# Kernel tuning notes

Measured on AMD Instinct MI355X. Metric: run time of the kernel, lower is better.

Reference implementation:

```python
import jax, jax.numpy as jnp
import numpy as np


def _edt2(mask):
    """Exact squared Euclidean distance transform of a bool [H,W] mask.

    Returns, per pixel, the squared distance to the nearest False pixel
    (0 where mask is False) -- same semantics as scipy distance_transform_edt^2.
    Pass 1: 1D nearest-zero distance along axis 0 (two scans).
    Pass 2: exact lower envelope along axis 1 via a vectorized min over columns.
    """
    H, W = mask.shape
    BIG = jnp.float32(H + W)  # 1D distance can never exceed H, acts as +inf

    def step(carry, m_row):  # carry: [W] running distance to last zero
        d = jnp.where(m_row, carry + 1.0, 0.0)
        return d, d

    init = jnp.full((W,), BIG, jnp.float32)
    _, fwd = jax.lax.scan(step, init, mask)
    _, bwd = jax.lax.scan(step, init, mask[::-1])
    g2 = jnp.minimum(fwd, bwd[::-1]) ** 2  # [H,W] squared 1D distances

    k = jnp.arange(W, dtype=jnp.float32)
    sq = (k[:, None] - k[None, :]) ** 2  # [Wj, Wk]
    # dt2[i,j] = min_k (j-k)^2 + g2[i,k]
    return jnp.min(g2[:, None, :] + sq[None, :, :], axis=-1)


def _dist_map(mask):
    # edt(pos) + edt(neg), then squared: cross term is 0 (supports disjoint),
    # so (edt_pos + edt_neg)^2 == edt_pos^2 + edt_neg^2 == edt2(pos) + edt2(neg).
    return _edt2(mask) + _edt2(~mask)


_dist_map_bc = jax.vmap(jax.vmap(_dist_map))  # over [B, C]


def setup_inputs() -> dict:
    key = jax.random.key(0)
    k1, k2 = jax.random.split(key)
    B, C, H, W = 8, 1, 256, 256
    inp = jax.random.normal(k1, (B, C, H, W), dtype=jnp.float32)
    target = jax.random.randint(k2, (B, C, H, W), 0, 2, dtype=jnp.int32)
    return {"inp": inp, "target": target}


def reference(inp, target):
    p = jax.nn.sigmoid(inp.astype(jnp.float32))      # [B,C,H,W]
    t = target.astype(jnp.float32)
    # distance maps computed on thresholded masks (no_grad in original)
    dist = _dist_map_bc(p > 0.5) + _dist_map_bc(t > 0.5)
    pred_error = (t - p) ** 2
    per_sample = jnp.mean(pred_error * dist, axis=(1, 2, 3))  # mean over c,x,y
    return jnp.mean(per_sample)[None]  # shape [1], matching FloatTensor(1)
```

## Files before the change

### kernel.cpp

```cpp
#include <hip/hip_runtime.h>


#define IMG 65536

__device__ __forceinline__ float g2_from_words(unsigned long long z0,
                                               unsigned long long z1,
                                               unsigned long long z2,
                                               unsigned long long z3,
                                               int i) {
    int wi = i >> 6, bi = i & 63;
    unsigned long long lowm  = (~0ULL) >> (63 - bi);
    unsigned long long highm = (~0ULL) << bi;
    unsigned long long z[4] = {z0, z1, z2, z3};

    int lz = -513;
    #pragma unroll
    for (int w = 0; w < 4; ++w) {
        unsigned long long m = z[w];
        if (w == wi) m &= lowm;
        if (w >  wi) m = 0;
        if (m) lz = (w << 6) + 63 - __clzll(m);
    }
    int fz = 768;
    #pragma unroll
    for (int w = 3; w >= 0; --w) {
        unsigned long long m = z[w];
        if (w == wi) m &= highm;
        if (w <  wi) m = 0;
        if (m) fz = (w << 6) + (__ffsll(m) - 1);
    }
    int u = i - lz, d = fz - i;
    float g = (float)(u < d ? u : d);
    return g * g;
}

__global__ __launch_bounds__(256) void build_masks(const float* __restrict__ inp,
                                                   const int* __restrict__ tgt,
                                                   unsigned short* __restrict__ PM,
                                                   float* __restrict__ out) {
    int bid = blockIdx.x;
    int w   = threadIdx.x;
    if (bid == 0 && w == 0) out[0] = 0.0f;

    int src = bid >> 7;
    int b   = (bid >> 4) & 7;
    int wd  = (bid >> 2) & 3;
    int q   = bid & 3;
    int h0  = (wd << 6) + (q << 4);
    int base = b * IMG + (h0 << 8) + w;

    unsigned int word = 0;
    if (src == 0) {
        #pragma unroll
        for (int hh = 0; hh < 16; ++hh)
            word |= ((unsigned int)(inp[base + (hh << 8)] > 0.0f)) << hh;
    } else {
        #pragma unroll
        for (int hh = 0; hh < 16; ++hh)
            word |= ((unsigned int)(tgt[base + (hh << 8)] > 0)) << hh;
    }
    PM[((((size_t)src * 8 + b) * 4 + wd) * 256 + w) * 4 + q] = (unsigned short)word;
}

__global__ __launch_bounds__(256) void envelope(const float* __restrict__ inp,
                                                const int* __restrict__ tgt,
                                                const unsigned long long* __restrict__ BM,
                                                float* __restrict__ out) {
    __shared__ float4 sg2[4][256];
    __shared__ float wsum[4];

    int b  = blockIdx.x >> 6;
    int r0 = (blockIdx.x & 63) << 2;
    int t  = threadIdx.x;

    {
        unsigned long long bp[4], bt[4];
        #pragma unroll
        for (int wd = 0; wd < 4; ++wd) {
            bp[wd] = BM[(((size_t)0 * 8 + b) * 4 + wd) * 256 + t];
            bt[wd] = BM[(((size_t)1 * 8 + b) * 4 + wd) * 256 + t];
        }
        #pragma unroll
        for (int rr = 0; rr < 4; ++rr) {
            int i = r0 + rr;
            float g0 = g2_from_words(~bp[0], ~bp[1], ~bp[2], ~bp[3], i);
            float g1 = g2_from_words( bp[0],  bp[1],  bp[2],  bp[3], i);
            float g2 = g2_from_words(~bt[0], ~bt[1], ~bt[2], ~bt[3], i);
            float g3 = g2_from_words( bt[0],  bt[1],  bt[2],  bt[3], i);
            sg2[rr][t] = make_float4(g0, g1, g2, g3);
        }
    }
    __syncthreads();

    int r  = t >> 6;
    int j0 = t & 63;
    float a[4][4];
    #pragma unroll
    for (int m = 0; m < 4; ++m)
        #pragma unroll
        for (int q = 0; q < 4; ++q) a[m][q] = 1e30f;

    #pragma unroll
    for (int kk = -2; kk <= 2; ++kk) {
        float s = (float)(kk * kk);
        #pragma unroll
        for (int q = 0; q < 4; ++q) {
            int k = j0 + (q << 6) + kk;
            k = min(max(k, 0), 255);
            float4 g = sg2[r][k];
            a[0][q] = fminf(a[0][q], g.x + s);
            a[1][q] = fminf(a[1][q], g.y + s);
            a[2][q] = fminf(a[2][q], g.z + s);
            a[3][q] = fminf(a[3][q], g.w + s);
        }
    }

    float U = 0.0f;
    #pragma unroll
    for (int m = 0; m < 4; ++m)
        #pragma unroll
        for (int q = 0; q < 4; ++q) U = fmaxf(U, a[m][q]);
    int R = (int)sqrtf(U) + 1;
    R = min(R, 255);
    #pragma unroll
    for (int off = 1; off < 64; off <<= 1) R = max(R, __shfl_xor(R, off));

    for (int kk = 3; kk <= R; ++kk) {
        float s = (float)(kk * kk);
        #pragma unroll
        for (int q = 0; q < 4; ++q) {
            int kl = max(j0 + (q << 6) - kk, 0);
            int kr = min(j0 + (q << 6) + kk, 255);
            float4 gl = sg2[r][kl];
            float4 gr = sg2[r][kr];
            a[0][q] = fminf(a[0][q], fminf(gl.x, gr.x) + s);
            a[1][q] = fminf(a[1][q], fminf(gl.y, gr.y) + s);
            a[2][q] = fminf(a[2][q], fminf(gl.z, gr.z) + s);
            a[3][q] = fminf(a[3][q], fminf(gl.w, gr.w) + s);
        }
    }

    int rowbase = b * IMG + ((r0 + r) << 8);
    float v = 0.0f;
    #pragma unroll
    for (int q = 0; q < 4; ++q) {
        int j = j0 + (q << 6);
        float dist = (a[0][q] + a[1][q]) + (a[2][q] + a[3][q]);
        float x  = inp[rowbase + j];
        float tt = (float)tgt[rowbase + j];
        float p  = 1.0f / (1.0f + __expf(-x));
        float e  = tt - p;
        v = fmaf(e * e, dist, v);
    }

    #pragma unroll
    for (int off = 32; off > 0; off >>= 1) v += __shfl_down(v, off);
    if ((t & 63) == 0) wsum[t >> 6] = v;
    __syncthreads();
    if (t == 0) {
        float s = (wsum[0] + wsum[1]) + (wsum[2] + wsum[3]);
        atomicAdd(out, s * (1.0f / 524288.0f));
    }
}

extern "C" void kernel_launch(void* const* d_in, const int* in_sizes, int n_in,
                              void* d_out, int out_size, void* d_ws, size_t ws_size,
                              hipStream_t stream) {
    const float* inp = (const float*)d_in[0];
    const int*   tgt = (const int*)d_in[1];
    unsigned short* PM = (unsigned short*)d_ws;
    const unsigned long long* BM = (const unsigned long long*)d_ws;
    float* out = (float*)d_out;

    build_masks<<<256, 256, 0, stream>>>(inp, tgt, PM, out);
    envelope<<<512, 256, 0, stream>>>(inp, tgt, BM, out);
}
```

Before: 68.03 us.

## Fuse mask build and envelope into one cooperative kernel with grid sync

Merges the bit-mask packing kernel and the distance envelope kernel into a single cooperative launch of 512 blocks. Each block first packs half of a 16-row slab into a byte mask, then a grid-wide sync precedes the envelope phase. This removes one kernel launch and the gap between launches. In exchange it pays for a grid barrier and a cooperative launch, and the mask writes become byte stores.

```diff
diff --git a/kernel.cpp b/kernel.cpp
--- a/kernel.cpp
+++ b/kernel.cpp
@@ -1,4 +1,7 @@
 #include <hip/hip_runtime.h>
+#include <hip/hip_cooperative_groups.h>
+
+namespace cg = cooperative_groups;
 
 
 #define IMG 65536
@@ -34,40 +37,45 @@
     return g * g;
 }
 
-__global__ __launch_bounds__(256) void build_masks(const float* __restrict__ inp,
-                                                   const int* __restrict__ tgt,
-                                                   unsigned short* __restrict__ PM,
-                                                   float* __restrict__ out) {
-    int bid = blockIdx.x;
-    int w   = threadIdx.x;
-    if (bid == 0 && w == 0) out[0] = 0.0f;
-
-    int src = bid >> 7;
-    int b   = (bid >> 4) & 7;
-    int wd  = (bid >> 2) & 3;
-    int q   = bid & 3;
-    int h0  = (wd << 6) + (q << 4);
-    int base = b * IMG + (h0 << 8) + w;
-
-    unsigned int word = 0;
-    if (src == 0) {
-        #pragma unroll
-        for (int hh = 0; hh < 16; ++hh)
-            word |= ((unsigned int)(inp[base + (hh << 8)] > 0.0f)) << hh;
-    } else {
-        #pragma unroll
-        for (int hh = 0; hh < 16; ++hh)
-            word |= ((unsigned int)(tgt[base + (hh << 8)] > 0)) << hh;
-    }
-    PM[((((size_t)src * 8 + b) * 4 + wd) * 256 + w) * 4 + q] = (unsigned short)word;
-}
-
-__global__ __launch_bounds__(256) void envelope(const float* __restrict__ inp,
-                                                const int* __restrict__ tgt,
-                                                const unsigned long long* __restrict__ BM,
-                                                float* __restrict__ out) {
+__global__ __launch_bounds__(256) void hddt_fused(const float* __restrict__ inp,
+                                                  const int* __restrict__ tgt,
+                                                  unsigned char* PM,
+                                                  const unsigned long long* BM,
+                                                  float* __restrict__ out) {
     __shared__ float4 sg2[4][256];
     __shared__ float wsum[4];
+
+    {
+        int bid = blockIdx.x;
+        int w   = threadIdx.x;
+        if (bid == 0 && w == 0)
+            __hip_atomic_store(out, 0.0f, __ATOMIC_RELAXED, __HIP_MEMORY_SCOPE_AGENT);
+
+        int task = bid >> 1;
+        int half = bid & 1;
+        int src  = task >> 7;
+        int b    = (task >> 4) & 7;
+        int wd   = (task >> 2) & 3;
+        int q    = task & 3;
+        int h0   = (wd << 6) + (q << 4) + (half << 3);
+        int base = b * IMG + (h0 << 8) + w;
+
+        unsigned int word = 0;
+        if (src == 0) {
+            #pragma unroll
+            for (int hh = 0; hh < 8; ++hh)
+                word |= ((unsigned int)(inp[base + (hh << 8)] > 0.0f)) << hh;
+        } else {
+            #pragma unroll
+            for (int hh = 0; hh < 8; ++hh)
+                word |= ((unsigned int)(tgt[base + (hh << 8)] > 0)) << hh;
+        }
+        PM[(((((size_t)src * 8 + b) * 4 + wd) * 256 + w) * 4 + q) * 2 + half] =
+            (unsigned char)word;
+    }
+
+    __threadfence();
+    cg::this_grid().sync();
 
     int b  = blockIdx.x >> 6;
     int r0 = (blockIdx.x & 63) << 2;
@@ -168,10 +176,11 @@
                               hipStream_t stream) {
     const float* inp = (const float*)d_in[0];
     const int*   tgt = (const int*)d_in[1];
-    unsigned short* PM = (unsigned short*)d_ws;
+    unsigned char* PM = (unsigned char*)d_ws;
     const unsigned long long* BM = (const unsigned long long*)d_ws;
     float* out = (float*)d_out;
 
-    build_masks<<<256, 256, 0, stream>>>(inp, tgt, PM, out);
-    envelope<<<512, 256, 0, stream>>>(inp, tgt, BM, out);
+    void* args[] = {(void*)&inp, (void*)&tgt, (void*)&PM, (void*)&BM, (void*)&out};
+    hipLaunchCooperativeKernel((const void*)hddt_fused, dim3(512), dim3(256),
+                               args, 0, stream);
 }
```

After: 181.4 us. 2.67x slower.
